# Kernel optimization log

Measured on AMD Instinct MI355X. Metric: run time of the kernel, lower is better.

Reference implementation:

```python
import jax, jax.numpy as jnp
import numpy as np

HEAD_SIZE = 64
NUM_HEADS = 16
D_MODEL = HEAD_SIZE * NUM_HEADS
BATCH = 2
SEQ = 2048


def setup_inputs() -> dict:
    key = jax.random.key(0)
    ks = jax.random.split(key, 9)
    s = 1.0 / np.sqrt(D_MODEL)
    inp = {
        "hidden_states": jax.random.normal(ks[0], (BATCH, SEQ, D_MODEL), jnp.float32),
        "Wq": jax.random.uniform(ks[1], (D_MODEL, D_MODEL), jnp.float32, -s, s),
        "bq": jax.random.uniform(ks[2], (D_MODEL,), jnp.float32, -s, s),
        "Wk": jax.random.uniform(ks[3], (D_MODEL, D_MODEL), jnp.float32, -s, s),
        "bk": jax.random.uniform(ks[4], (D_MODEL,), jnp.float32, -s, s),
        "Wv": jax.random.uniform(ks[5], (D_MODEL, D_MODEL), jnp.float32, -s, s),
        "bv": jax.random.uniform(ks[6], (D_MODEL,), jnp.float32, -s, s),
        "Wo": jax.random.uniform(ks[7], (D_MODEL, D_MODEL), jnp.float32, -s, s),
        "bo": jax.random.uniform(ks[8], (D_MODEL,), jnp.float32, -s, s),
    }
    return inp


def _split_heads(x):
    # [B, S, H*D] -> [B, H, S, D]
    b, s, _ = x.shape
    return x.reshape(b, s, NUM_HEADS, HEAD_SIZE).transpose(0, 2, 1, 3)


def reference(hidden_states, Wq, bq, Wk, bk, Wv, bv, Wo, bo):
    q = _split_heads(hidden_states @ Wq + bq)  # [B,H,S,D]
    k = _split_heads(hidden_states @ Wk + bk)
    v = _split_heads(hidden_states @ Wv + bv)
    scale = 1.0 / jnp.sqrt(jnp.asarray(HEAD_SIZE, hidden_states.dtype))
    scores = jnp.einsum("bhqd,bhkd->bhqk", q, k) * scale  # [B,H,S,S]
    weights = jax.nn.softmax(scores, axis=-1)
    attended = jnp.einsum("bhqk,bhkd->bhqd", weights, v)  # [B,H,S,D]
    merged = attended.transpose(0, 2, 1, 3).reshape(hidden_states.shape)  # [B,S,H*D]
    return merged @ Wo + bo
```

## Files before the change

### kernel.cpp

```cpp
#include <hip/hip_runtime.h>
#include <hip/hip_bf16.h>

#define D_MODEL 1024
#define HEADS 16
#define HSZ 64
#define BATCH 2
#define SEQ 2048
#define TOK (BATCH*SEQ)
#define NT (SEQ/64)

typedef __attribute__((ext_vector_type(8))) short bf16x8;
typedef __attribute__((ext_vector_type(4))) float f32x4;

#define QSCALE 0.1803368801111244f
#define THR_L2 11.541560327f

static __device__ __forceinline__ unsigned short f2bf(float f) {
  union { float f; unsigned u; } v; v.f = f;
  unsigned r = v.u + 0x7fffu + ((v.u >> 16) & 1u);
  return (unsigned short)(r >> 16);
}

static __device__ __forceinline__ float exp2_fast(float x) {
  float r;
  asm("v_exp_f32 %0, %1" : "=v"(r) : "v"(x));
  return r;
}

static __device__ __forceinline__ unsigned cvt_pk_bf16(float a, float b) {
  unsigned r;
  asm("v_cvt_pk_bf16_f32 %0, %1, %2" : "=v"(r) : "v"(a), "v"(b));
  return r;
}

static __device__ __forceinline__ int swz128(int row, int g) {
  return ((row << 7) + (g << 4)) ^ ((row & 7) << 4);
}

static __device__ __forceinline__ void load_lds16(const void* g, void* l) {
  __builtin_amdgcn_global_load_lds(
      (const __attribute__((address_space(1))) unsigned*)g,
      (__attribute__((address_space(3))) unsigned*)l, 16, 0, 0);
}


__global__ void cvt_bf16_kernel(const float* __restrict__ src,
                                unsigned short* __restrict__ dst, int n) {
  int i = (blockIdx.x * blockDim.x + threadIdx.x) * 8;
  if (i >= n) return;
  float4 v0 = *reinterpret_cast<const float4*>(src + i);
  float4 v1 = *reinterpret_cast<const float4*>(src + i + 4);
  ushort4 o0, o1;
  o0.x = f2bf(v0.x); o0.y = f2bf(v0.y); o0.z = f2bf(v0.z); o0.w = f2bf(v0.w);
  o1.x = f2bf(v1.x); o1.y = f2bf(v1.y); o1.z = f2bf(v1.z); o1.w = f2bf(v1.w);
  *reinterpret_cast<ushort4*>(dst + i) = o0;
  *reinterpret_cast<ushort4*>(dst + i + 4) = o1;
}

__global__ void transpose_cvt_kernel(const float* __restrict__ Wq, const float* __restrict__ Wk,
                                     const float* __restrict__ Wv, const float* __restrict__ Wo,
                                     unsigned short* __restrict__ Wqkvt,
                                     unsigned short* __restrict__ Wot) {
  __shared__ float tile[32][33];
  int m = blockIdx.z;
  const float* src = (m == 0) ? Wq : (m == 1) ? Wk : (m == 2) ? Wv : Wo;
  unsigned short* dst = (m < 3) ? (Wqkvt + (size_t)m * D_MODEL * D_MODEL) : Wot;
  int i0 = blockIdx.y * 32, o0 = blockIdx.x * 32;
  int tx = threadIdx.x, ty = threadIdx.y;
  for (int k = 0; k < 32; k += 8)
    tile[ty + k][tx] = src[(size_t)(i0 + ty + k) * D_MODEL + o0 + tx];
  __syncthreads();
  for (int k = 0; k < 32; k += 8)
    dst[(size_t)(o0 + ty + k) * D_MODEL + i0 + tx] = f2bf(tile[tx][ty + k]);
}


template<int EPI>
__global__ __launch_bounds__(256) void gemm128_kernel(
    const unsigned short* __restrict__ A, const unsigned short* __restrict__ Bt,
    int K, int N,
    const float* __restrict__ b0, const float* __restrict__ b1, const float* __restrict__ b2,
    unsigned short* __restrict__ Qb, unsigned short* __restrict__ Kb,
    unsigned short* __restrict__ Vtb, float* __restrict__ Cout)
{
  __shared__ char As[128 * 64];
  __shared__ char Bs[128 * 64];
  int m0 = blockIdx.y * 128, n0 = blockIdx.x * 128;
  int tid = threadIdx.x;
  int wv = tid >> 6, l = tid & 63;
  int wm = wv >> 1, wn = wv & 1;
  int lg = l >> 4, lr = l & 15;
  int srow = wv * 32 + (l >> 2);
  int scol = (l & 3) * 8;

  f32x4 acc[4][4];
#pragma unroll
  for (int i = 0; i < 4; i++)
#pragma unroll
    for (int j = 0; j < 4; j++) acc[i][j] = (f32x4){0.f, 0.f, 0.f, 0.f};

  for (int k0 = 0; k0 < K; k0 += 32) {
    __syncthreads();
    const unsigned short* ga = A  + (size_t)(m0 + srow) * K + k0 + scol;
    const unsigned short* gb = Bt + (size_t)(n0 + srow) * K + k0 + scol;
    load_lds16(ga,                       As + wv * 2048);
    load_lds16(ga + (size_t)16 * K,      As + wv * 2048 + 1024);
    load_lds16(gb,                       Bs + wv * 2048);
    load_lds16(gb + (size_t)16 * K,      Bs + wv * 2048 + 1024);
    __syncthreads();

    bf16x8 af[4], bfv[4];
#pragma unroll
    for (int mi = 0; mi < 4; mi++)
      af[mi] = *reinterpret_cast<const bf16x8*>(As + (wm * 64 + mi * 16 + lr) * 64 + lg * 16);
#pragma unroll
    for (int ni = 0; ni < 4; ni++)
      bfv[ni] = *reinterpret_cast<const bf16x8*>(Bs + (wn * 64 + ni * 16 + lr) * 64 + lg * 16);
#pragma unroll
    for (int mi = 0; mi < 4; mi++)
#pragma unroll
      for (int ni = 0; ni < 4; ni++)
        acc[mi][ni] = __builtin_amdgcn_mfma_f32_16x16x32_bf16(af[mi], bfv[ni], acc[mi][ni], 0, 0, 0);
  }

#pragma unroll
  for (int mi = 0; mi < 4; mi++) {
    int gr0 = m0 + wm * 64 + mi * 16 + lg * 4;
#pragma unroll
    for (int ni = 0; ni < 4; ni++) {
      int gc = n0 + wn * 64 + ni * 16 + lr;
      if (EPI == 0) {
        int mat = gc >> 10, o = gc & 1023;
        int hh = o >> 6, d = o & 63;
        const float* bias = (mat == 0) ? b0 : (mat == 1) ? b1 : b2;
        float bv = bias[o];
#pragma unroll
        for (int r = 0; r < 4; r++) {
          int t = gr0 + r;
          int b = t >> 11, s = t & 2047;
          float v = acc[mi][ni][r] + bv;
          if (mat == 0) v *= QSCALE;
          unsigned short u = f2bf(v);
          size_t head = (size_t)(b * HEADS + hh);
          if (mat == 0)      Qb [(head * SEQ + s) * HSZ + d] = u;
          else if (mat == 1) Kb [(head * SEQ + s) * HSZ + d] = u;
          else               Vtb[(head * HSZ + d) * SEQ + s] = u;
        }
      } else {
        float bv = b0[gc];
#pragma unroll
        for (int r = 0; r < 4; r++) {
          int t = gr0 + r;
          Cout[(size_t)t * N + gc] = acc[mi][ni][r] + bv;
        }
      }
    }
  }
}


__global__ __launch_bounds__(256, 2) void attn_kernel(
    const unsigned short* __restrict__ Qb, const unsigned short* __restrict__ Kb,
    const unsigned short* __restrict__ Vtb, unsigned short* __restrict__ Mg)
{
  __shared__ char Ks[64 * 128];
  __shared__ char Vs[64 * 128];
  __shared__ char Ps[4][32 * 128];

  int orig = blockIdx.y * 16 + blockIdx.x;
  int swzb = (orig & 7) * 64 + (orig >> 3);
  int bh = swzb >> 4;
  int q0 = (swzb & 15) * 128;
  int b = bh >> 4, h = bh & 15;
  int tid = threadIdx.x, w = tid >> 6, l = tid & 63;
  int lg = l >> 4, lr = l & 15;
  const unsigned short* Qh = Qb + (size_t)bh * SEQ * HSZ;
  const unsigned short* Kh = Kb + (size_t)bh * SEQ * HSZ;
  const unsigned short* Vh = Vtb + (size_t)bh * HSZ * SEQ;

  bf16x8 qfr[2][2];
#pragma unroll
  for (int qf = 0; qf < 2; qf++)
#pragma unroll
    for (int k2 = 0; k2 < 2; k2++)
      qfr[qf][k2] = *reinterpret_cast<const bf16x8*>(
          Qh + (size_t)(q0 + w * 32 + qf * 16 + lr) * HSZ + k2 * 32 + lg * 8);

  f32x4 of[2][4];
  f32x4 lones[2];
#pragma unroll
  for (int qf = 0; qf < 2; qf++) {
    lones[qf] = (f32x4){0.f, 0.f, 0.f, 0.f};
#pragma unroll
    for (int ni = 0; ni < 4; ni++) of[qf][ni] = (f32x4){0.f, 0.f, 0.f, 0.f};
  }
  float m0r = -1e30f, m1r = -1e30f;

  bf16x8 vone;
#pragma unroll
  for (int j = 0; j < 8; j++) vone[j] = (short)0x3F80;

  int srow = tid >> 3, sg = tid & 7;

  uint4 ka  = *reinterpret_cast<const uint4*>(Kh + (size_t)srow * HSZ + sg * 8);
  uint4 kb2 = *reinterpret_cast<const uint4*>(Kh + (size_t)(srow + 32) * HSZ + sg * 8);
  uint4 va  = *reinterpret_cast<const uint4*>(Vh + (size_t)srow * SEQ + sg * 8);
  uint4 vb2 = *reinterpret_cast<const uint4*>(Vh + (size_t)(srow + 32) * SEQ + sg * 8);

  for (int kt = 0; kt < NT; ++kt) {
    __syncthreads();
    *reinterpret_cast<uint4*>(Ks + swz128(srow,      sg)) = ka;
    *reinterpret_cast<uint4*>(Ks + swz128(srow + 32, sg)) = kb2;
    *reinterpret_cast<uint4*>(Vs + swz128(srow,      sg)) = va;
    *reinterpret_cast<uint4*>(Vs + swz128(srow + 32, sg)) = vb2;
    __syncthreads();

    if (kt + 1 < NT) {
      const unsigned short* Kn = Kh + (size_t)(kt + 1) * 64 * HSZ;
      const unsigned short* Vn = Vh + (kt + 1) * 64;
      ka  = *reinterpret_cast<const uint4*>(Kn + (size_t)srow * HSZ + sg * 8);
      kb2 = *reinterpret_cast<const uint4*>(Kn + (size_t)(srow + 32) * HSZ + sg * 8);
      va  = *reinterpret_cast<const uint4*>(Vn + (size_t)srow * SEQ + sg * 8);
      vb2 = *reinterpret_cast<const uint4*>(Vn + (size_t)(srow + 32) * SEQ + sg * 8);
    }

    bf16x8 kf[4][2];
#pragma unroll
    for (int ni = 0; ni < 4; ni++)
#pragma unroll
      for (int k2 = 0; k2 < 2; k2++)
        kf[ni][k2] = *reinterpret_cast<const bf16x8*>(Ks + swz128(ni * 16 + lr, k2 * 4 + lg));

    f32x4 sf[2][4];
#pragma unroll
    for (int qf = 0; qf < 2; qf++)
#pragma unroll
      for (int ni = 0; ni < 4; ni++) {
        sf[qf][ni] = (f32x4){0.f, 0.f, 0.f, 0.f};
#pragma unroll
        for (int k2 = 0; k2 < 2; k2++)
          sf[qf][ni] = __builtin_amdgcn_mfma_f32_16x16x32_bf16(kf[ni][k2], qfr[qf][k2], sf[qf][ni], 0, 0, 0);
      }

    float lm0 = fmaxf(fmaxf(fmaxf(sf[0][0][0], sf[0][0][1]), fmaxf(sf[0][0][2], sf[0][0][3])),
                      fmaxf(fmaxf(sf[0][1][0], sf[0][1][1]), fmaxf(sf[0][1][2], sf[0][1][3])));
    lm0 = fmaxf(lm0,
          fmaxf(fmaxf(fmaxf(sf[0][2][0], sf[0][2][1]), fmaxf(sf[0][2][2], sf[0][2][3])),
                fmaxf(fmaxf(sf[0][3][0], sf[0][3][1]), fmaxf(sf[0][3][2], sf[0][3][3]))));
    float lm1 = fmaxf(fmaxf(fmaxf(sf[1][0][0], sf[1][0][1]), fmaxf(sf[1][0][2], sf[1][0][3])),
                      fmaxf(fmaxf(sf[1][1][0], sf[1][1][1]), fmaxf(sf[1][1][2], sf[1][1][3])));
    lm1 = fmaxf(lm1,
          fmaxf(fmaxf(fmaxf(sf[1][2][0], sf[1][2][1]), fmaxf(sf[1][2][2], sf[1][2][3])),
                fmaxf(fmaxf(sf[1][3][0], sf[1][3][1]), fmaxf(sf[1][3][2], sf[1][3][3]))));

    int grow = (lm0 > m0r + THR_L2) || (lm1 > m1r + THR_L2);
    if (__any(grow)) {
      float vm0 = fmaxf(lm0, __shfl_xor(lm0, 16));
      vm0 = fmaxf(vm0, __shfl_xor(vm0, 32));
      float vm1 = fmaxf(lm1, __shfl_xor(lm1, 16));
      vm1 = fmaxf(vm1, __shfl_xor(vm1, 32));
      float mn0 = fmaxf(m0r, vm0), mn1 = fmaxf(m1r, vm1);
      float al0 = exp2_fast(m0r - mn0), al1 = exp2_fast(m1r - mn1);
      m0r = mn0; m1r = mn1;
#pragma unroll
      for (int r = 0; r < 4; r++) {
        float a0 = __shfl(al0, lg * 4 + r, 16);
        float a1 = __shfl(al1, lg * 4 + r, 16);
        lones[0][r] *= a0; lones[1][r] *= a1;
#pragma unroll
        for (int ni = 0; ni < 4; ni++) { of[0][ni][r] *= a0; of[1][ni][r] *= a1; }
      }
    }

#pragma unroll
    for (int qf = 0; qf < 2; qf++) {
      float mq = qf ? m1r : m0r;
      int prow = qf * 16 + lr;
#pragma unroll
      for (int ni = 0; ni < 4; ni++) {
        float p0 = exp2_fast(sf[qf][ni][0] - mq);
        float p1 = exp2_fast(sf[qf][ni][1] - mq);
        float p2 = exp2_fast(sf[qf][ni][2] - mq);
        float p3 = exp2_fast(sf[qf][ni][3] - mq);
        uint2 pw;
        pw.x = cvt_pk_bf16(p0, p1);
        pw.y = cvt_pk_bf16(p2, p3);
        int off = ((prow << 7) + (ni << 5) + (lg << 3)) ^ ((prow & 7) << 4);
        *reinterpret_cast<uint2*>(Ps[w] + off) = pw;
      }
    }

    bf16x8 vf[4][2];
#pragma unroll
    for (int ni = 0; ni < 4; ni++)
#pragma unroll
      for (int k2 = 0; k2 < 2; k2++)
        vf[ni][k2] = *reinterpret_cast<const bf16x8*>(Vs + swz128(ni * 16 + lr, k2 * 4 + lg));
    bf16x8 pa[2][2];
#pragma unroll
    for (int qf = 0; qf < 2; qf++)
#pragma unroll
      for (int k2 = 0; k2 < 2; k2++)
        pa[qf][k2] = *reinterpret_cast<const bf16x8*>(Ps[w] + swz128(qf * 16 + lr, k2 * 4 + lg));
#pragma unroll
    for (int qf = 0; qf < 2; qf++) {
#pragma unroll
      for (int k2 = 0; k2 < 2; k2++)
        lones[qf] = __builtin_amdgcn_mfma_f32_16x16x32_bf16(pa[qf][k2], vone, lones[qf], 0, 0, 0);
#pragma unroll
      for (int ni = 0; ni < 4; ni++)
#pragma unroll
        for (int k2 = 0; k2 < 2; k2++)
          of[qf][ni] = __builtin_amdgcn_mfma_f32_16x16x32_bf16(pa[qf][k2], vf[ni][k2], of[qf][ni], 0, 0, 0);
    }
  }

#pragma unroll
  for (int qf = 0; qf < 2; qf++)
#pragma unroll
    for (int r = 0; r < 4; r++) {
      float inv = 1.0f / lones[qf][r];
      int q = q0 + w * 32 + qf * 16 + lg * 4 + r;
#pragma unroll
      for (int ni = 0; ni < 4; ni++) {
        int dm = h * 64 + ni * 16 + lr;
        Mg[(size_t)(b * SEQ + q) * D_MODEL + dm] = f2bf(of[qf][ni][r] * inv);
      }
    }
}


extern "C" void kernel_launch(void* const* d_in, const int* in_sizes, int n_in,
                              void* d_out, int out_size, void* d_ws, size_t ws_size,
                              hipStream_t stream) {
  const float* X  = (const float*)d_in[0];
  const float* Wq = (const float*)d_in[1];
  const float* bq = (const float*)d_in[2];
  const float* Wk = (const float*)d_in[3];
  const float* bk = (const float*)d_in[4];
  const float* Wv = (const float*)d_in[5];
  const float* bv = (const float*)d_in[6];
  const float* Wo = (const float*)d_in[7];
  const float* bo = (const float*)d_in[8];
  float* out = (float*)d_out;

  char* ws = (char*)d_ws;
  unsigned short* Xbf   = (unsigned short*)(ws);
  unsigned short* Wqkvt = (unsigned short*)(ws + ((size_t)8  << 20));
  unsigned short* Wot   = (unsigned short*)(ws + ((size_t)14 << 20));
  unsigned short* Qb    = (unsigned short*)(ws + ((size_t)16 << 20));
  unsigned short* Kb    = (unsigned short*)(ws + ((size_t)24 << 20));
  unsigned short* Vtb   = (unsigned short*)(ws + ((size_t)32 << 20));
  unsigned short* Mg = Xbf;

  cvt_bf16_kernel<<<(TOK * D_MODEL / 8 + 255) / 256, 256, 0, stream>>>(X, Xbf, TOK * D_MODEL);
  transpose_cvt_kernel<<<dim3(32, 32, 4), dim3(32, 8), 0, stream>>>(Wq, Wk, Wv, Wo, Wqkvt, Wot);
  gemm128_kernel<0><<<dim3(24, 32), 256, 0, stream>>>(Xbf, Wqkvt, 1024, 3072,
                                                      bq, bk, bv, Qb, Kb, Vtb, nullptr);
  attn_kernel<<<dim3(16, 32), 256, 0, stream>>>(Qb, Kb, Vtb, Mg);
  gemm128_kernel<1><<<dim3(8, 32), 256, 0, stream>>>(Mg, Wot, 1024, 1024,
                                                     bo, nullptr, nullptr,
                                                     nullptr, nullptr, nullptr, out);
}
```

Measured before the change: 211.3 us.

## Split attention block into 8 waves of 16 query rows each

```diff
diff --git a/kernel.cpp b/kernel.cpp
--- a/kernel.cpp
+++ b/kernel.cpp
@@ -35,6 +35,10 @@
 
 static __device__ __forceinline__ int swz128(int row, int g) {
   return ((row << 7) + (g << 4)) ^ ((row & 7) << 4);
+}
+
+static __device__ __forceinline__ int xs4(int lr) {
+  return ((lr & 7) << 1) | (lr >> 3);
 }
 
 static __device__ __forceinline__ void load_lds16(const void* g, void* l) {
@@ -159,13 +163,13 @@
 }
 
 
-__global__ __launch_bounds__(256, 2) void attn_kernel(
+__global__ __launch_bounds__(512, 4) void attn_kernel(
     const unsigned short* __restrict__ Qb, const unsigned short* __restrict__ Kb,
     const unsigned short* __restrict__ Vtb, unsigned short* __restrict__ Mg)
 {
   __shared__ char Ks[64 * 128];
   __shared__ char Vs[64 * 128];
-  __shared__ char Ps[4][32 * 128];
+  __shared__ char Ps[8][16 * 128];
 
   int orig = blockIdx.y * 16 + blockIdx.x;
   int swzb = (orig & 7) * 64 + (orig >> 3);
@@ -178,23 +182,18 @@
   const unsigned short* Kh = Kb + (size_t)bh * SEQ * HSZ;
   const unsigned short* Vh = Vtb + (size_t)bh * HSZ * SEQ;
 
-  bf16x8 qfr[2][2];
-#pragma unroll
-  for (int qf = 0; qf < 2; qf++)
-#pragma unroll
-    for (int k2 = 0; k2 < 2; k2++)
-      qfr[qf][k2] = *reinterpret_cast<const bf16x8*>(
-          Qh + (size_t)(q0 + w * 32 + qf * 16 + lr) * HSZ + k2 * 32 + lg * 8);
-
-  f32x4 of[2][4];
-  f32x4 lones[2];
-#pragma unroll
-  for (int qf = 0; qf < 2; qf++) {
-    lones[qf] = (f32x4){0.f, 0.f, 0.f, 0.f};
-#pragma unroll
-    for (int ni = 0; ni < 4; ni++) of[qf][ni] = (f32x4){0.f, 0.f, 0.f, 0.f};
-  }
-  float m0r = -1e30f, m1r = -1e30f;
+  bf16x8 qf2[2];
+#pragma unroll
+  for (int k2 = 0; k2 < 2; k2++)
+    qf2[k2] = *reinterpret_cast<const bf16x8*>(
+        Qh + (size_t)(q0 + w * 16 + lr) * HSZ + k2 * 32 + lg * 8);
+
+  f32x4 of[4];
+  f32x4 lones;
+#pragma unroll
+  for (int ni = 0; ni < 4; ni++) of[ni] = (f32x4){0.f, 0.f, 0.f, 0.f};
+  lones = (f32x4){0.f, 0.f, 0.f, 0.f};
+  float m_r = -1e30f;
 
   bf16x8 vone;
 #pragma unroll
@@ -202,131 +201,99 @@
 
   int srow = tid >> 3, sg = tid & 7;
 
-  uint4 ka  = *reinterpret_cast<const uint4*>(Kh + (size_t)srow * HSZ + sg * 8);
-  uint4 kb2 = *reinterpret_cast<const uint4*>(Kh + (size_t)(srow + 32) * HSZ + sg * 8);
-  uint4 va  = *reinterpret_cast<const uint4*>(Vh + (size_t)srow * SEQ + sg * 8);
-  uint4 vb2 = *reinterpret_cast<const uint4*>(Vh + (size_t)(srow + 32) * SEQ + sg * 8);
+  uint4 ka = *reinterpret_cast<const uint4*>(Kh + (size_t)srow * HSZ + sg * 8);
+  uint4 va = *reinterpret_cast<const uint4*>(Vh + (size_t)srow * SEQ + sg * 8);
 
   for (int kt = 0; kt < NT; ++kt) {
     __syncthreads();
-    *reinterpret_cast<uint4*>(Ks + swz128(srow,      sg)) = ka;
-    *reinterpret_cast<uint4*>(Ks + swz128(srow + 32, sg)) = kb2;
-    *reinterpret_cast<uint4*>(Vs + swz128(srow,      sg)) = va;
-    *reinterpret_cast<uint4*>(Vs + swz128(srow + 32, sg)) = vb2;
+    *reinterpret_cast<uint4*>(Ks + swz128(srow, sg)) = ka;
+    *reinterpret_cast<uint4*>(Vs + swz128(srow, sg)) = va;
     __syncthreads();
 
     if (kt + 1 < NT) {
-      const unsigned short* Kn = Kh + (size_t)(kt + 1) * 64 * HSZ;
-      const unsigned short* Vn = Vh + (kt + 1) * 64;
-      ka  = *reinterpret_cast<const uint4*>(Kn + (size_t)srow * HSZ + sg * 8);
-      kb2 = *reinterpret_cast<const uint4*>(Kn + (size_t)(srow + 32) * HSZ + sg * 8);
-      va  = *reinterpret_cast<const uint4*>(Vn + (size_t)srow * SEQ + sg * 8);
-      vb2 = *reinterpret_cast<const uint4*>(Vn + (size_t)(srow + 32) * SEQ + sg * 8);
-    }
-
-    bf16x8 kf[4][2];
+      ka = *reinterpret_cast<const uint4*>(Kh + (size_t)((kt + 1) * 64 + srow) * HSZ + sg * 8);
+      va = *reinterpret_cast<const uint4*>(Vh + (size_t)srow * SEQ + (kt + 1) * 64 + sg * 8);
+    }
+
+    f32x4 sf[4];
+#pragma unroll
+    for (int ni = 0; ni < 4; ni++) {
+      sf[ni] = (f32x4){0.f, 0.f, 0.f, 0.f};
+#pragma unroll
+      for (int k2 = 0; k2 < 2; k2++) {
+        bf16x8 kf = *reinterpret_cast<const bf16x8*>(Ks + swz128(ni * 16 + lr, k2 * 4 + lg));
+        sf[ni] = __builtin_amdgcn_mfma_f32_16x16x32_bf16(kf, qf2[k2], sf[ni], 0, 0, 0);
+      }
+    }
+
+    float lm = fmaxf(fmaxf(fmaxf(sf[0][0], sf[0][1]), fmaxf(sf[0][2], sf[0][3])),
+                     fmaxf(fmaxf(sf[1][0], sf[1][1]), fmaxf(sf[1][2], sf[1][3])));
+    lm = fmaxf(lm,
+         fmaxf(fmaxf(fmaxf(sf[2][0], sf[2][1]), fmaxf(sf[2][2], sf[2][3])),
+               fmaxf(fmaxf(sf[3][0], sf[3][1]), fmaxf(sf[3][2], sf[3][3]))));
+
+    if (__any(lm > m_r + THR_L2)) {
+      float vm = fmaxf(lm, __shfl_xor(lm, 16));
+      vm = fmaxf(vm, __shfl_xor(vm, 32));
+      float mn = fmaxf(m_r, vm);
+      float al = exp2_fast(m_r - mn);
+      m_r = mn;
+#pragma unroll
+      for (int r = 0; r < 4; r++) {
+        float a = __shfl(al, lg * 4 + r, 16);
+        lones[r] *= a;
+#pragma unroll
+        for (int ni = 0; ni < 4; ni++) of[ni][r] *= a;
+      }
+    }
+
+#pragma unroll
+    for (int ni = 0; ni < 4; ni++) {
+      float p0 = exp2_fast(sf[ni][0] - m_r);
+      float p1 = exp2_fast(sf[ni][1] - m_r);
+      float p2 = exp2_fast(sf[ni][2] - m_r);
+      float p3 = exp2_fast(sf[ni][3] - m_r);
+      uint2 pw;
+      pw.x = cvt_pk_bf16(p0, p1);
+      pw.y = cvt_pk_bf16(p2, p3);
+      int slot = (ni * 4 + lg) ^ xs4(lr);
+      *reinterpret_cast<uint2*>(Ps[w] + (lr << 7) + (slot << 3)) = pw;
+    }
+
+    bf16x8 pa[2];
+#pragma unroll
+    for (int k2 = 0; k2 < 2; k2++) {
+      int g0 = k2 * 8 + lg * 2;
+      uint2 lo = *reinterpret_cast<const uint2*>(Ps[w] + (lr << 7) + (((g0)     ^ xs4(lr)) << 3));
+      uint2 hi = *reinterpret_cast<const uint2*>(Ps[w] + (lr << 7) + (((g0 + 1) ^ xs4(lr)) << 3));
+      int4 t = {(int)lo.x, (int)lo.y, (int)hi.x, (int)hi.y};
+      pa[k2] = *reinterpret_cast<bf16x8*>(&t);
+    }
+
+    __builtin_amdgcn_s_setprio(1);
+#pragma unroll
+    for (int k2 = 0; k2 < 2; k2++)
+      lones = __builtin_amdgcn_mfma_f32_16x16x32_bf16(pa[k2], vone, lones, 0, 0, 0);
 #pragma unroll
     for (int ni = 0; ni < 4; ni++)
 #pragma unroll
-      for (int k2 = 0; k2 < 2; k2++)
-        kf[ni][k2] = *reinterpret_cast<const bf16x8*>(Ks + swz128(ni * 16 + lr, k2 * 4 + lg));
-
-    f32x4 sf[2][4];
-#pragma unroll
-    for (int qf = 0; qf < 2; qf++)
-#pragma unroll
-      for (int ni = 0; ni < 4; ni++) {
-        sf[qf][ni] = (f32x4){0.f, 0.f, 0.f, 0.f};
-#pragma unroll
-        for (int k2 = 0; k2 < 2; k2++)
-          sf[qf][ni] = __builtin_amdgcn_mfma_f32_16x16x32_bf16(kf[ni][k2], qfr[qf][k2], sf[qf][ni], 0, 0, 0);
+      for (int k2 = 0; k2 < 2; k2++) {
+        bf16x8 vf = *reinterpret_cast<const bf16x8*>(Vs + swz128(ni * 16 + lr, k2 * 4 + lg));
+        of[ni] = __builtin_amdgcn_mfma_f32_16x16x32_bf16(pa[k2], vf, of[ni], 0, 0, 0);
       }
-
-    float lm0 = fmaxf(fmaxf(fmaxf(sf[0][0][0], sf[0][0][1]), fmaxf(sf[0][0][2], sf[0][0][3])),
-                      fmaxf(fmaxf(sf[0][1][0], sf[0][1][1]), fmaxf(sf[0][1][2], sf[0][1][3])));
-    lm0 = fmaxf(lm0,
-          fmaxf(fmaxf(fmaxf(sf[0][2][0], sf[0][2][1]), fmaxf(sf[0][2][2], sf[0][2][3])),
-                fmaxf(fmaxf(sf[0][3][0], sf[0][3][1]), fmaxf(sf[0][3][2], sf[0][3][3]))));
-    float lm1 = fmaxf(fmaxf(fmaxf(sf[1][0][0], sf[1][0][1]), fmaxf(sf[1][0][2], sf[1][0][3])),
-                      fmaxf(fmaxf(sf[1][1][0], sf[1][1][1]), fmaxf(sf[1][1][2], sf[1][1][3])));
-    lm1 = fmaxf(lm1,
-          fmaxf(fmaxf(fmaxf(sf[1][2][0], sf[1][2][1]), fmaxf(sf[1][2][2], sf[1][2][3])),
-                fmaxf(fmaxf(sf[1][3][0], sf[1][3][1]), fmaxf(sf[1][3][2], sf[1][3][3]))));
-
-    int grow = (lm0 > m0r + THR_L2) || (lm1 > m1r + THR_L2);
-    if (__any(grow)) {
-      float vm0 = fmaxf(lm0, __shfl_xor(lm0, 16));
-      vm0 = fmaxf(vm0, __shfl_xor(vm0, 32));
-      float vm1 = fmaxf(lm1, __shfl_xor(lm1, 16));
-      vm1 = fmaxf(vm1, __shfl_xor(vm1, 32));
-      float mn0 = fmaxf(m0r, vm0), mn1 = fmaxf(m1r, vm1);
-      float al0 = exp2_fast(m0r - mn0), al1 = exp2_fast(m1r - mn1);
-      m0r = mn0; m1r = mn1;
-#pragma unroll
-      for (int r = 0; r < 4; r++) {
-        float a0 = __shfl(al0, lg * 4 + r, 16);
-        float a1 = __shfl(al1, lg * 4 + r, 16);
-        lones[0][r] *= a0; lones[1][r] *= a1;
-#pragma unroll
-        for (int ni = 0; ni < 4; ni++) { of[0][ni][r] *= a0; of[1][ni][r] *= a1; }
-      }
-    }
-
-#pragma unroll
-    for (int qf = 0; qf < 2; qf++) {
-      float mq = qf ? m1r : m0r;
-      int prow = qf * 16 + lr;
-#pragma unroll
-      for (int ni = 0; ni < 4; ni++) {
-        float p0 = exp2_fast(sf[qf][ni][0] - mq);
-        float p1 = exp2_fast(sf[qf][ni][1] - mq);
-        float p2 = exp2_fast(sf[qf][ni][2] - mq);
-        float p3 = exp2_fast(sf[qf][ni][3] - mq);
-        uint2 pw;
-        pw.x = cvt_pk_bf16(p0, p1);
-        pw.y = cvt_pk_bf16(p2, p3);
-        int off = ((prow << 7) + (ni << 5) + (lg << 3)) ^ ((prow & 7) << 4);
-        *reinterpret_cast<uint2*>(Ps[w] + off) = pw;
-      }
-    }
-
-    bf16x8 vf[4][2];
-#pragma unroll
-    for (int ni = 0; ni < 4; ni++)
-#pragma unroll
-      for (int k2 = 0; k2 < 2; k2++)
-        vf[ni][k2] = *reinterpret_cast<const bf16x8*>(Vs + swz128(ni * 16 + lr, k2 * 4 + lg));
-    bf16x8 pa[2][2];
-#pragma unroll
-    for (int qf = 0; qf < 2; qf++)
-#pragma unroll
-      for (int k2 = 0; k2 < 2; k2++)
-        pa[qf][k2] = *reinterpret_cast<const bf16x8*>(Ps[w] + swz128(qf * 16 + lr, k2 * 4 + lg));
-#pragma unroll
-    for (int qf = 0; qf < 2; qf++) {
-#pragma unroll
-      for (int k2 = 0; k2 < 2; k2++)
-        lones[qf] = __builtin_amdgcn_mfma_f32_16x16x32_bf16(pa[qf][k2], vone, lones[qf], 0, 0, 0);
-#pragma unroll
-      for (int ni = 0; ni < 4; ni++)
-#pragma unroll
-        for (int k2 = 0; k2 < 2; k2++)
-          of[qf][ni] = __builtin_amdgcn_mfma_f32_16x16x32_bf16(pa[qf][k2], vf[ni][k2], of[qf][ni], 0, 0, 0);
-    }
+    __builtin_amdgcn_s_setprio(0);
   }
 
 #pragma unroll
-  for (int qf = 0; qf < 2; qf++)
-#pragma unroll
-    for (int r = 0; r < 4; r++) {
-      float inv = 1.0f / lones[qf][r];
-      int q = q0 + w * 32 + qf * 16 + lg * 4 + r;
-#pragma unroll
-      for (int ni = 0; ni < 4; ni++) {
-        int dm = h * 64 + ni * 16 + lr;
-        Mg[(size_t)(b * SEQ + q) * D_MODEL + dm] = f2bf(of[qf][ni][r] * inv);
-      }
-    }
+  for (int r = 0; r < 4; r++) {
+    float inv = 1.0f / lones[r];
+    int q = q0 + w * 16 + lg * 4 + r;
+#pragma unroll
+    for (int ni = 0; ni < 4; ni++) {
+      int dm = h * 64 + ni * 16 + lr;
+      Mg[(size_t)(b * SEQ + q) * D_MODEL + dm] = f2bf(of[ni][r] * inv);
+    }
+  }
 }
 
 
@@ -357,7 +324,7 @@
   transpose_cvt_kernel<<<dim3(32, 32, 4), dim3(32, 8), 0, stream>>>(Wq, Wk, Wv, Wo, Wqkvt, Wot);
   gemm128_kernel<0><<<dim3(24, 32), 256, 0, stream>>>(Xbf, Wqkvt, 1024, 3072,
                                                       bq, bk, bv, Qb, Kb, Vtb, nullptr);
-  attn_kernel<<<dim3(16, 32), 256, 0, stream>>>(Qb, Kb, Vtb, Mg);
+  attn_kernel<<<dim3(16, 32), 512, 0, stream>>>(Qb, Kb, Vtb, Mg);
   gemm128_kernel<1><<<dim3(8, 32), 256, 0, stream>>>(Mg, Wot, 1024, 1024,
                                                      bo, nullptr, nullptr,
                                                      nullptr, nullptr, nullptr, out);
```

Result: no change. 209.0 us (-1.1%).
